# Optimization experiments

Measured on AMD Instinct MI355X. Metric: run time of the kernel, lower is better.

The kernel has to match this reference:

```python
import jax, jax.numpy as jnp
import numpy as np
import math

B, S, DIM, H, HD = 2, 2048, 2048, 16, 128


def _rotary(t, cos, sin):
    # t: [B, S, H, HD]; cos/sin: [S, HD//2]
    tr = t.reshape(*t.shape[:-1], HD // 2, 2)
    t_re, t_im = tr[..., 0], tr[..., 1]
    c = cos[None, :, None, :]
    s = sin[None, :, None, :]
    o_re = t_re * c - t_im * s
    o_im = t_re * s + t_im * c
    out = jnp.stack([o_re, o_im], axis=-1)
    return out.reshape(t.shape)


def setup_inputs() -> dict:
    key = jax.random.key(0)
    ks = jax.random.split(key, 6)
    x = jax.random.normal(ks[0], (B, S, DIM), dtype=jnp.float32)
    # rotary frequencies (base 10000), matching complex freqs_cis = exp(i * t * freq)
    inv_freq = 1.0 / (10000.0 ** (np.arange(0, HD, 2, dtype=np.float32) / HD))
    t = np.arange(S, dtype=np.float32)
    ang = np.outer(t, inv_freq)  # [S, HD//2]
    freqs_cos = jnp.asarray(np.cos(ang), dtype=jnp.float32)
    freqs_sin = jnp.asarray(np.sin(ang), dtype=jnp.float32)
    # causal boolean mask [1,1,S,S]
    mask = jnp.tril(jnp.ones((S, S), dtype=bool))[None, None]
    scale = 0.02
    qw = jax.random.normal(ks[1], (DIM, H * HD), dtype=jnp.float32) * scale
    kw = jax.random.normal(ks[2], (DIM, H * HD), dtype=jnp.float32) * scale
    vw = jax.random.normal(ks[3], (DIM, H * HD), dtype=jnp.float32) * scale
    ow = jax.random.normal(ks[4], (H * HD, DIM), dtype=jnp.float32) * scale
    return {"x": x, "freqs_cos": freqs_cos, "freqs_sin": freqs_sin, "mask": mask,
            "qw": qw, "kw": kw, "vw": vw, "ow": ow}


def reference(x, freqs_cos, freqs_sin, mask, qw, kw, vw, ow):
    bsz, slen, _ = x.shape
    q = (x @ qw).reshape(bsz, slen, H, HD)
    k = (x @ kw).reshape(bsz, slen, H, HD)
    v = (x @ vw).reshape(bsz, slen, H, HD)
    q = _rotary(q, freqs_cos[:slen], freqs_sin[:slen])
    k = _rotary(k, freqs_cos[:slen], freqs_sin[:slen])
    # [B, H, S, HD]
    q = q.transpose(0, 2, 1, 3)
    k = k.transpose(0, 2, 1, 3)
    v = v.transpose(0, 2, 1, 3)
    scale = 1.0 / math.sqrt(HD)
    scores = jnp.einsum('bhqd,bhkd->bhqk', q, k) * scale
    neg_inf = jnp.finfo(scores.dtype).min
    scores = jnp.where(mask, scores, neg_inf)
    attn_w = jax.nn.softmax(scores, axis=-1)
    attn = jnp.einsum('bhqk,bhkd->bhqd', attn_w, v)
    attn = attn.transpose(0, 2, 1, 3).reshape(bsz, slen, H * HD)
    out = attn @ ow
    return (out, attn_w)
```

## Files before the change

### kernel.cpp

```cpp
#include <hip/hip_runtime.h>
#include <stdint.h>

#define S 2048
#define DIMM 2048
#define NH 16
#define HD 128
#define NB 2
#define M4 4096

typedef unsigned short u16;
typedef unsigned int u32;
typedef __attribute__((ext_vector_type(8))) short short8;
typedef __attribute__((ext_vector_type(4))) float f32x4;

__device__ __forceinline__ u16 f2bf(float f) {
  union { float f; u32 u; } v; v.f = f;
  u32 u = v.u + 0x7fffu + ((v.u >> 16) & 1u);
  return (u16)(u >> 16);
}
__device__ __forceinline__ float bf2f(u16 b) {
  union { u32 u; float f; } v; v.u = ((u32)b) << 16;
  return v.f;
}
__device__ __forceinline__ u32 cvt_pk_bf16(float lo, float hi) {
  u32 r; asm("v_cvt_pk_bf16_f32 %0, %1, %2" : "=v"(r) : "v"(lo), "v"(hi)); return r;
}
__device__ __forceinline__ void gl_lds16(const void* g, void* l) {
  __builtin_amdgcn_global_load_lds((const __attribute__((address_space(1))) void*)g,
                                   (__attribute__((address_space(3))) void*)l, 16, 0, 0);
}
#define MFMA16(a, b, c) __builtin_amdgcn_mfma_f32_16x16x32_bf16(a, b, c, 0, 0, 0)

__global__ __launch_bounds__(256) void k_conv_x(const float* __restrict__ x, u16* __restrict__ xb) {
  int i = (blockIdx.x * 256 + threadIdx.x) * 8;
  float4 a = *(const float4*)&x[i];
  float4 b = *(const float4*)&x[i + 4];
  uint4 o;
  o.x = (u32)f2bf(a.x) | ((u32)f2bf(a.y) << 16);
  o.y = (u32)f2bf(a.z) | ((u32)f2bf(a.w) << 16);
  o.z = (u32)f2bf(b.x) | ((u32)f2bf(b.y) << 16);
  o.w = (u32)f2bf(b.z) | ((u32)f2bf(b.w) << 16);
  *(uint4*)&xb[i] = o;
}

__global__ __launch_bounds__(256) void k_transpose_w4(const float* __restrict__ w0, const float* __restrict__ w1,
                                                      const float* __restrict__ w2, const float* __restrict__ w3,
                                                      u16* __restrict__ t0, u16* __restrict__ t1,
                                                      u16* __restrict__ t2, u16* __restrict__ t3) {
  __shared__ u16 t[64][72];
  int zi = blockIdx.z;
  const float* w = (zi == 0) ? w0 : (zi == 1) ? w1 : (zi == 2) ? w2 : w3;
  u16* wt = (zi == 0) ? t0 : (zi == 1) ? t1 : (zi == 2) ? t2 : t3;
  int k0 = blockIdx.y * 64, n0 = blockIdx.x * 64;
  int tid = threadIdx.x;
  int r0 = tid >> 4, c4 = (tid & 15) * 4;
#pragma unroll
  for (int p = 0; p < 4; ++p) {
    int r = r0 + p * 16;
    float4 v = *(const float4*)&w[(size_t)(k0 + r) * DIMM + n0 + c4];
    t[c4 + 0][r] = f2bf(v.x); t[c4 + 1][r] = f2bf(v.y);
    t[c4 + 2][r] = f2bf(v.z); t[c4 + 3][r] = f2bf(v.w);
  }
  __syncthreads();
#pragma unroll
  for (int p = 0; p < 2; ++p) {
    int cc = tid + p * 256;
    int rn = cc >> 3, ck = (cc & 7) * 8;
    *(uint4*)&wt[(size_t)(n0 + rn) * DIMM + k0 + ck] = *(const uint4*)&t[rn][ck];
  }
}

__device__ __forceinline__ void gemm128_core(const u16* __restrict__ A, const u16* __restrict__ Bt,
                                             int m0, int n0, int Kd, u16* lA, u16* lB,
                                             f32x4 acc[4][4]) {
  int tid = threadIdx.x;
  int lane = tid & 63;
  int wid = tid >> 6;
  int wm = wid >> 1, wn = wid & 1;
  int c0 = tid, c1 = tid + 256;
  int a_r0 = c0 >> 2, a_k0 = (c0 & 3) * 8;
  int a_r1 = c1 >> 2, a_k1 = (c1 & 3) * 8;
  int ln = lane & 15, sub = lane >> 4;
  for (int kt = 0; kt < Kd; kt += 32) {
    gl_lds16(&A[(size_t)(m0 + a_r0) * Kd + kt + a_k0], &lA[c0 * 8]);
    gl_lds16(&A[(size_t)(m0 + a_r1) * Kd + kt + a_k1], &lA[c1 * 8]);
    gl_lds16(&Bt[(size_t)(n0 + a_r0) * Kd + kt + a_k0], &lB[c0 * 8]);
    gl_lds16(&Bt[(size_t)(n0 + a_r1) * Kd + kt + a_k1], &lB[c1 * 8]);
    __syncthreads();
    short8 af[4], bf[4];
#pragma unroll
    for (int mf = 0; mf < 4; ++mf)
      af[mf] = *(const short8*)&lA[(wm * 64 + mf * 16 + ln) * 32 + sub * 8];
#pragma unroll
    for (int nf = 0; nf < 4; ++nf)
      bf[nf] = *(const short8*)&lB[(wn * 64 + nf * 16 + ln) * 32 + sub * 8];
#pragma unroll
    for (int mf = 0; mf < 4; ++mf)
#pragma unroll
      for (int nf = 0; nf < 4; ++nf)
        acc[mf][nf] = MFMA16(af[mf], bf[nf], acc[mf][nf]);
    __syncthreads();
  }
}

__global__ __launch_bounds__(256) void k_gemm_qkv(const u16* __restrict__ xb,
                                                  const u16* __restrict__ qwT, const u16* __restrict__ kwT,
                                                  const u16* __restrict__ vwT,
                                                  const float* __restrict__ fc, const float* __restrict__ fs,
                                                  u16* __restrict__ qws, u16* __restrict__ kws,
                                                  u16* __restrict__ vtws, float* __restrict__ aw_all) {
  __shared__ u16 lA[128 * 32], lB[128 * 32];
  int f = blockIdx.y * 48 + blockIdx.x;
  int fp = (f & 7) * 192 + (f >> 3);
  int bx = fp % 48, byy = fp / 48;

  {
    int tid = threadIdx.x;
    f32x4 zf = {0.f, 0.f, 0.f, 0.f};
#pragma unroll
    for (int z = 0; z < 11; ++z) {
      int t = f * 11 + z;
      if (t < 15872) {
        int head = t / 496;
        int r = t - head * 496;
        int a = 0;
#pragma unroll
        for (int q = 30; q >= 1; --q) {
          if (r >= q * (63 - q) / 2) { a = q; break; }
        }
        int j = r - a * (63 - a) / 2;
        int kt = a + 1 + j;
        float* base = aw_all + (size_t)head * S * S + (size_t)(a * 64) * S + kt * 64;
#pragma unroll
        for (int i = 0; i < 4; ++i) {
          int c = i * 256 + tid;
          int row = c >> 4, col = (c & 15) * 4;
          __builtin_nontemporal_store(zf, (f32x4*)&base[(size_t)row * S + col]);
        }
      }
    }
  }

  int region = bx >> 4;
  const u16* Bt = (region == 0) ? qwT : ((region == 1) ? kwT : vwT);
  int n0 = (bx & 15) * 128;
  int m0 = byy * 128;
  f32x4 acc[4][4];
  f32x4 z4 = {0.f, 0.f, 0.f, 0.f};
#pragma unroll
  for (int i = 0; i < 4; ++i)
#pragma unroll
    for (int j = 0; j < 4; ++j) acc[i][j] = z4;
  gemm128_core(xb, Bt, m0, n0, DIMM, lA, lB, acc);
  int lane = threadIdx.x & 63, wid = threadIdx.x >> 6;
  int wm = wid >> 1, wn = wid & 1;
  int ln = lane & 15, sub = lane >> 4;
  if (region == 2) {
#pragma unroll
    for (int mf = 0; mf < 4; ++mf)
#pragma unroll
      for (int nf = 0; nf < 4; ++nf) {
        int m = m0 + wm * 64 + mf * 16 + sub * 4;
        int nl = n0 + wn * 64 + nf * 16 + ln;
        int b = m >> 11, s = m & 2047;
        int h = nl >> 7, d = nl & 127;
        u32 w0 = cvt_pk_bf16(acc[mf][nf][0], acc[mf][nf][1]);
        u32 w1 = cvt_pk_bf16(acc[mf][nf][2], acc[mf][nf][3]);
        uint2 pw = {w0, w1};
        *(uint2*)&vtws[((size_t)((b << 4) + h) * HD + d) * S + s] = pw;
      }
  } else {
    u16* dst = (region == 0) ? qws : kws;
#pragma unroll
    for (int mf = 0; mf < 4; ++mf)
#pragma unroll
      for (int nf = 0; nf < 4; ++nf) {
        int mbase = m0 + wm * 64 + mf * 16 + sub * 4;
        int nl = n0 + wn * 64 + nf * 16 + ln;
        int h = nl >> 7, d = nl & 127;
        int pi = d >> 1;
#pragma unroll
        for (int r = 0; r < 4; ++r) {
          int m = mbase + r;
          int b = m >> 11, s = m & 2047;
          float c = fc[s * 64 + pi];
          float sn = fs[s * 64 + pi];
          float v = acc[mf][nf][r];
          float prt = __shfl_xor(v, 1);
          float o = (ln & 1) ? (prt * sn + v * c) : (v * c - prt * sn);
          float o2 = __shfl_xor(o, 1);
          if (!(ln & 1)) {
            u32 opk = cvt_pk_bf16(o, o2);
            *(u32*)&dst[((size_t)((b << 4) + h) * S + s) * HD + d] = opk;
          }
        }
      }
  }
}

__global__ __launch_bounds__(256, 4) void k_attn(const u16* __restrict__ qws, const u16* __restrict__ kws,
                                                 const u16* __restrict__ vtws,
                                                 float* __restrict__ aw_all, u16* __restrict__ att) {
  __shared__ u16 lK[2][32 * 128];
  __shared__ u16 lV[2][128 * 32];
  __shared__ u16 lP[64 * 32];

  int f = blockIdx.x;
  int x = f & 7;
  int j = f >> 3;
  int cu = j & 31;
  int u = j >> 5;
  int by = 4 * x + u;
  int c2 = (u & 2) ? ((cu + 16) & 31) : cu;
  int qt = (u & 1) ? (31 - c2) : c2;
  int b = by >> 4, h = by & 15;
  const u16* qb = qws + (size_t)by * S * HD;
  const u16* kb = kws + (size_t)by * S * HD;
  const u16* vb = vtws + (size_t)by * HD * S;
  float* aw = aw_all + (size_t)by * S * S;
  int tid = threadIdx.x, lane = tid & 63, w = tid >> 6;
  int sub = lane >> 4, ln = lane & 15;
  int l7 = ln & 7, l3 = ln & 3;
  int q0 = qt * 64;
  int qrow = w * 16 + ln;
  int nkt = 2 * qt + 2;
  const float SC = 0.08838834764831845f * 1.4426950408889634f;

  auto stageK = [&](int kt, int bs) {
#pragma unroll
    for (int i = 0; i < 2; ++i) {
      int c = tid + i * 256;
      int row = c >> 4, p = c & 15;
      gl_lds16(&kb[(size_t)(kt * 32 + row) * HD + ((p ^ (row & 7)) << 3)], &lK[bs][c * 8]);
    }
  };
  auto stageV = [&](int kt, int bs) {
#pragma unroll
    for (int i = 0; i < 2; ++i) {
      int c = tid + i * 256;
      int row = c >> 2, p = c & 3;
      gl_lds16(&vb[(size_t)row * S + kt * 32 + ((p ^ (row & 3)) << 3)], &lV[bs][c * 8]);
    }
  };

  u16* lVlin = &lV[0][0];
#pragma unroll
  for (int i = 0; i < 4; ++i) {
    int c = tid + i * 256;
    int row = c >> 4, p = c & 15;
    gl_lds16(&qb[(size_t)(q0 + row) * HD + ((p ^ (row & 7)) << 3)], &lVlin[c * 8]);
  }
  stageK(0, 0);
  __syncthreads();

  short8 qf[4];
#pragma unroll
  for (int ks = 0; ks < 4; ++ks)
    qf[ks] = *(const short8*)&lVlin[qrow * 128 + (((ks * 4 + sub) ^ l7) << 3)];

  float ts = 0.f;
  for (int kt = 0; kt < nkt; ++kt) {
    int cur = kt & 1;
    if (kt + 1 < nkt) stageK(kt + 1, cur ^ 1);
    f32x4 sacc[2];
#pragma unroll
    for (int nf = 0; nf < 2; ++nf) sacc[nf] = f32x4{0.f, 0.f, 0.f, 0.f};
    __builtin_amdgcn_s_setprio(1);
#pragma unroll
    for (int nf = 0; nf < 2; ++nf) {
      int krow = nf * 16 + ln;
#pragma unroll
      for (int ks = 0; ks < 4; ++ks) {
        short8 kf = *(const short8*)&lK[cur][krow * 128 + (((ks * 4 + sub) ^ l7) << 3)];
        sacc[nf] = MFMA16(kf, qf[ks], sacc[nf]);
      }
    }
    __builtin_amdgcn_s_setprio(0);
    bool msk = (kt >= 2 * qt);
#pragma unroll
    for (int nf = 0; nf < 2; ++nf)
#pragma unroll
      for (int r = 0; r < 4; ++r) {
        float zz = sacc[nf][r] * SC;
        bool dead = msk && (kt * 32 + nf * 16 + sub * 4 + r > q0 + qrow);
        if (!dead) ts += exp2f(zz);
      }
    __syncthreads();
  }
  ts += __shfl_xor(ts, 16);
  ts += __shfl_xor(ts, 32);
  float mb = __log2f(ts);

  f32x4 oacc[8];
#pragma unroll
  for (int i = 0; i < 8; ++i) oacc[i] = f32x4{0.f, 0.f, 0.f, 0.f};
  stageK(nkt - 1, 0);
  stageV(nkt - 1, 0);
  __syncthreads();
  for (int it = 0; it < nkt; ++it) {
    int kt = nkt - 1 - it;
    int cur = it & 1;
    if (it + 1 < nkt) { stageK(kt - 1, cur ^ 1); stageV(kt - 1, cur ^ 1); }
    f32x4 sacc[2];
#pragma unroll
    for (int nf = 0; nf < 2; ++nf) sacc[nf] = f32x4{0.f, 0.f, 0.f, 0.f};
    __builtin_amdgcn_s_setprio(1);
#pragma unroll
    for (int nf = 0; nf < 2; ++nf) {
      int krow = nf * 16 + ln;
#pragma unroll
      for (int ks = 0; ks < 4; ++ks) {
        short8 kf = *(const short8*)&lK[cur][krow * 128 + (((ks * 4 + sub) ^ l7) << 3)];
        sacc[nf] = MFMA16(kf, qf[ks], sacc[nf]);
      }
    }
    __builtin_amdgcn_s_setprio(0);
    bool msk = (kt >= 2 * qt);
#pragma unroll
    for (int nf = 0; nf < 2; ++nf) {
      float p0 = exp2f(sacc[nf][0] * SC - mb);
      float p1 = exp2f(sacc[nf][1] * SC - mb);
      float p2 = exp2f(sacc[nf][2] * SC - mb);
      float p3 = exp2f(sacc[nf][3] * SC - mb);
      if (msk) {
        int base = kt * 32 + nf * 16 + sub * 4 - (q0 + qrow);
        if (base + 0 > 0) p0 = 0.f;
        if (base + 1 > 0) p1 = 0.f;
        if (base + 2 > 0) p2 = 0.f;
        if (base + 3 > 0) p3 = 0.f;
      }
      f32x4 pv = {p0, p1, p2, p3};
      __builtin_nontemporal_store(pv, (f32x4*)&aw[(size_t)(q0 + qrow) * S + kt * 32 + nf * 16 + sub * 4]);
      u32 w0 = cvt_pk_bf16(p0, p1);
      u32 w1 = cvt_pk_bf16(p2, p3);
      uint2 pw = {w0, w1};
      int c16 = (2 * nf + (sub >> 1)) ^ l3;
      *(uint2*)&lP[qrow * 32 + (c16 << 3) + ((sub & 1) << 2)] = pw;
    }
    short8 pa = *(const short8*)&lP[qrow * 32 + ((sub ^ l3) << 3)];
    __builtin_amdgcn_s_setprio(1);
#pragma unroll
    for (int nf2 = 0; nf2 < 8; ++nf2) {
      int drow = nf2 * 16 + ln;
      short8 vv = *(const short8*)&lV[cur][drow * 32 + ((sub ^ (drow & 3)) << 3)];
      oacc[nf2] = MFMA16(vv, pa, oacc[nf2]);
    }
    __builtin_amdgcn_s_setprio(0);
    __syncthreads();
  }

#pragma unroll
  for (int nf2 = 0; nf2 < 8; ++nf2) {
    u32 w0 = cvt_pk_bf16(oacc[nf2][0], oacc[nf2][1]);
    u32 w1 = cvt_pk_bf16(oacc[nf2][2], oacc[nf2][3]);
    uint2 ow2 = {w0, w1};
    *(uint2*)&att[(size_t)(b * S + q0 + qrow) * (NH * HD) + h * 128 + nf2 * 16 + sub * 4] = ow2;
  }
}

__global__ __launch_bounds__(256) void k_gemm_out(const u16* __restrict__ att, const u16* __restrict__ owT,
                                                  float* __restrict__ out) {
  __shared__ u16 lA[128 * 32], lB[128 * 32];
  int f = blockIdx.y * 16 + blockIdx.x;
  int fp = (f & 7) * 64 + (f >> 3);
  int n0 = (fp & 15) * 128, m0 = (fp >> 4) * 128;
  f32x4 acc[4][4];
  f32x4 z4 = {0.f, 0.f, 0.f, 0.f};
#pragma unroll
  for (int i = 0; i < 4; ++i)
#pragma unroll
    for (int j = 0; j < 4; ++j) acc[i][j] = z4;
  gemm128_core(att, owT, m0, n0, DIMM, lA, lB, acc);
  int lane = threadIdx.x & 63, wid = threadIdx.x >> 6;
  int wm = wid >> 1, wn = wid & 1;
  int ln = lane & 15, sub = lane >> 4;
#pragma unroll
  for (int mf = 0; mf < 4; ++mf)
#pragma unroll
    for (int nf = 0; nf < 4; ++nf)
#pragma unroll
      for (int r = 0; r < 4; ++r) {
        int m = m0 + wm * 64 + mf * 16 + sub * 4 + r;
        int nl = n0 + wn * 64 + nf * 16 + ln;
        out[(size_t)m * DIMM + nl] = acc[mf][nf][r];
      }
}

extern "C" void kernel_launch(void* const* d_in, const int* in_sizes, int n_in,
                              void* d_out, int out_size, void* d_ws, size_t ws_size,
                              hipStream_t stream) {
  const float* x  = (const float*)d_in[0];
  const float* fc = (const float*)d_in[1];
  const float* fs = (const float*)d_in[2];
  const float* qw = (const float*)d_in[4];
  const float* kw = (const float*)d_in[5];
  const float* vw = (const float*)d_in[6];
  const float* ow = (const float*)d_in[7];
  float* out = (float*)d_out;
  float* aw  = out + (size_t)M4 * DIMM;

  char* wsb = (char*)d_ws;
  u16* xb   = (u16*)(wsb);
  u16* qwT  = (u16*)(wsb + (size_t)16 * 1024 * 1024);
  u16* kwT  = (u16*)(wsb + (size_t)24 * 1024 * 1024);
  u16* vwT  = (u16*)(wsb + (size_t)32 * 1024 * 1024);
  u16* owT  = (u16*)(wsb + (size_t)40 * 1024 * 1024);
  u16* qws  = (u16*)(wsb + (size_t)48 * 1024 * 1024);
  u16* kws  = (u16*)(wsb + (size_t)64 * 1024 * 1024);
  u16* vtws = (u16*)(wsb + (size_t)80 * 1024 * 1024);
  u16* att  = (u16*)(wsb + (size_t)96 * 1024 * 1024);

  k_conv_x<<<4096, 256, 0, stream>>>(x, xb);
  k_transpose_w4<<<dim3(32, 32, 4), 256, 0, stream>>>(qw, kw, vw, ow, qwT, kwT, vwT, owT);
  k_gemm_qkv<<<dim3(48, 32), 256, 0, stream>>>(xb, qwT, kwT, vwT, fc, fs, qws, kws, vtws, aw);
  k_attn<<<1024, 256, 0, stream>>>(qws, kws, vtws, aw, att);
  k_gemm_out<<<dim3(16, 32), 256, 0, stream>>>(att, owT, out);
}
```

Baseline: 392.7 us.

## Rewrite projection GEMMs as 8-wave 128x256 double-buffered pipelined tiles

Replaces the single-buffered 128x128, 4-wave GEMM core with an 8-wave 128x256 tile that has a K-step of 64 and double-buffered LDS. It also XOR-swizzles the LDS layout to avoid bank conflicts and interleaves the prefetch of the next tile with MFMA work using explicit waitcnt, barriers and setprio. The QKV and output projection kernels are relaunched with fewer, larger blocks, and the masked attention-weight zeroing work is redistributed across them. The intent is to hide global-load latency and raise MFMA utilisation. The cost is more LDS per block (96KB), which limits occupancy, and fewer blocks for the output GEMM (256).

```diff
diff --git a/kernel.cpp b/kernel.cpp
--- a/kernel.cpp
+++ b/kernel.cpp
@@ -70,56 +70,136 @@
   }
 }
 
-__device__ __forceinline__ void gemm128_core(const u16* __restrict__ A, const u16* __restrict__ Bt,
-                                             int m0, int n0, int Kd, u16* lA, u16* lB,
-                                             f32x4 acc[4][4]) {
+__device__ __forceinline__ void gemm8p(const u16* __restrict__ A, const u16* __restrict__ Bt,
+                                       int m0, int n0,
+                                       u16 (*smA)[128 * 64], u16 (*smB)[256 * 64],
+                                       f32x4 acc[4][4]) {
   int tid = threadIdx.x;
-  int lane = tid & 63;
-  int wid = tid >> 6;
-  int wm = wid >> 1, wn = wid & 1;
-  int c0 = tid, c1 = tid + 256;
-  int a_r0 = c0 >> 2, a_k0 = (c0 & 3) * 8;
-  int a_r1 = c1 >> 2, a_k1 = (c1 & 3) * 8;
+  int lane = tid & 63, wid = tid >> 6;
+  int wm = wid >> 2, wn = wid & 3;
   int ln = lane & 15, sub = lane >> 4;
-  for (int kt = 0; kt < Kd; kt += 32) {
-    gl_lds16(&A[(size_t)(m0 + a_r0) * Kd + kt + a_k0], &lA[c0 * 8]);
-    gl_lds16(&A[(size_t)(m0 + a_r1) * Kd + kt + a_k1], &lA[c1 * 8]);
-    gl_lds16(&Bt[(size_t)(n0 + a_r0) * Kd + kt + a_k0], &lB[c0 * 8]);
-    gl_lds16(&Bt[(size_t)(n0 + a_r1) * Kd + kt + a_k1], &lB[c1 * 8]);
-    __syncthreads();
-    short8 af[4], bf[4];
-#pragma unroll
-    for (int mf = 0; mf < 4; ++mf)
-      af[mf] = *(const short8*)&lA[(wm * 64 + mf * 16 + ln) * 32 + sub * 8];
+
+  auto stageA = [&](int t, int bs) {
+    int kk = t << 6;
+#pragma unroll
+    for (int i = 0; i < 2; ++i) {
+      int c = tid + i * 512;
+      int row = c >> 3, p = c & 7;
+      gl_lds16(&A[(size_t)(m0 + row) * DIMM + kk + ((p ^ (row & 7)) << 3)],
+               &smA[bs][(row << 6) + (p << 3)]);
+    }
+  };
+  auto stageB = [&](int t, int bs) {
+    int kk = t << 6;
+#pragma unroll
+    for (int i = 0; i < 4; ++i) {
+      int c = tid + i * 512;
+      int row = c >> 3, p = c & 7;
+      gl_lds16(&Bt[(size_t)(n0 + row) * DIMM + kk + ((p ^ (row & 7)) << 3)],
+               &smB[bs][(row << 6) + (p << 3)]);
+    }
+  };
+  auto rdA = [&](int bs, int mf, int ks) -> short8 {
+    int row = (wm << 6) + (mf << 4) + ln;
+    return *(const short8*)&smA[bs][(row << 6) + ((((ks << 2) + sub) ^ (row & 7)) << 3)];
+  };
+  auto rdB = [&](int bs, int nf, int ks) -> short8 {
+    int row = (wn << 6) + (nf << 4) + ln;
+    return *(const short8*)&smB[bs][(row << 6) + ((((ks << 2) + sub) ^ (row & 7)) << 3)];
+  };
+
+  stageA(0, 0); stageB(0, 0);
+  asm volatile("s_waitcnt vmcnt(0)" ::: "memory");
+  __syncthreads();
+
+  const int nt = DIMM / 64;
+  for (int t = 0; t < nt; ++t) {
+    int cur = t & 1, nb = cur ^ 1;
+    bool pf = (t + 1 < nt);
+    short8 bfr[4][2];
+    if (pf) {
+      stageA(t + 1, nb);
+      asm volatile("s_waitcnt vmcnt(2)" ::: "memory");
+    } else {
+      asm volatile("s_waitcnt vmcnt(0)" ::: "memory");
+    }
+    __builtin_amdgcn_s_barrier();
+    __builtin_amdgcn_sched_barrier(0);
 #pragma unroll
     for (int nf = 0; nf < 4; ++nf)
-      bf[nf] = *(const short8*)&lB[(wn * 64 + nf * 16 + ln) * 32 + sub * 8];
-#pragma unroll
-    for (int mf = 0; mf < 4; ++mf)
-#pragma unroll
-      for (int nf = 0; nf < 4; ++nf)
-        acc[mf][nf] = MFMA16(af[mf], bf[nf], acc[mf][nf]);
-    __syncthreads();
-  }
-}
-
-__global__ __launch_bounds__(256) void k_gemm_qkv(const u16* __restrict__ xb,
-                                                  const u16* __restrict__ qwT, const u16* __restrict__ kwT,
-                                                  const u16* __restrict__ vwT,
-                                                  const float* __restrict__ fc, const float* __restrict__ fs,
-                                                  u16* __restrict__ qws, u16* __restrict__ kws,
-                                                  u16* __restrict__ vtws, float* __restrict__ aw_all) {
-  __shared__ u16 lA[128 * 32], lB[128 * 32];
-  int f = blockIdx.y * 48 + blockIdx.x;
-  int fp = (f & 7) * 192 + (f >> 3);
-  int bx = fp % 48, byy = fp / 48;
+#pragma unroll
+      for (int ks = 0; ks < 2; ++ks) bfr[nf][ks] = rdB(cur, nf, ks);
+    {
+      short8 a00 = rdA(cur, 0, 0), a01 = rdA(cur, 0, 1);
+      short8 a10 = rdA(cur, 1, 0), a11 = rdA(cur, 1, 1);
+      asm volatile("s_waitcnt lgkmcnt(0)" ::: "memory");
+      __builtin_amdgcn_sched_barrier(0);
+      __builtin_amdgcn_s_setprio(1);
+#pragma unroll
+      for (int nf = 0; nf < 4; ++nf) {
+        acc[0][nf] = MFMA16(a00, bfr[nf][0], acc[0][nf]);
+        acc[0][nf] = MFMA16(a01, bfr[nf][1], acc[0][nf]);
+        acc[1][nf] = MFMA16(a10, bfr[nf][0], acc[1][nf]);
+        acc[1][nf] = MFMA16(a11, bfr[nf][1], acc[1][nf]);
+      }
+      __builtin_amdgcn_s_setprio(0);
+    }
+    __builtin_amdgcn_s_barrier();
+    __builtin_amdgcn_sched_barrier(0);
+    {
+      short8 a00 = rdA(cur, 2, 0), a01 = rdA(cur, 2, 1);
+      short8 a10 = rdA(cur, 3, 0), a11 = rdA(cur, 3, 1);
+      if (pf) stageB(t + 1, nb);
+      __builtin_amdgcn_s_barrier();
+      asm volatile("s_waitcnt lgkmcnt(0)" ::: "memory");
+      __builtin_amdgcn_sched_barrier(0);
+      __builtin_amdgcn_s_setprio(1);
+#pragma unroll
+      for (int nf = 0; nf < 4; ++nf) {
+        acc[2][nf] = MFMA16(a00, bfr[nf][0], acc[2][nf]);
+        acc[2][nf] = MFMA16(a01, bfr[nf][1], acc[2][nf]);
+        acc[3][nf] = MFMA16(a10, bfr[nf][0], acc[3][nf]);
+        acc[3][nf] = MFMA16(a11, bfr[nf][1], acc[3][nf]);
+      }
+      __builtin_amdgcn_s_setprio(0);
+    }
+    asm volatile("s_waitcnt lgkmcnt(0)" ::: "memory");
+    __builtin_amdgcn_s_barrier();
+    __builtin_amdgcn_sched_barrier(0);
+  }
+}
+
+__global__ __launch_bounds__(512, 2) void k_gemm_qkv8(const u16* __restrict__ xb,
+                                                      const u16* __restrict__ qwT, const u16* __restrict__ kwT,
+                                                      const u16* __restrict__ vwT,
+                                                      const float* __restrict__ fc, const float* __restrict__ fs,
+                                                      u16* __restrict__ qws, u16* __restrict__ kws,
+                                                      u16* __restrict__ vtws, float* __restrict__ aw_all) {
+  __shared__ u16 smA[2][128 * 64];
+  __shared__ u16 smB[2][256 * 64];
+  int tid = threadIdx.x;
+  int f = blockIdx.x;
+  int fp = (f & 7) * 96 + (f >> 3);
+  int bx = fp % 24, by = fp / 24;
+  int region = bx >> 3;
+  const u16* Bt = (region == 0) ? qwT : ((region == 1) ? kwT : vwT);
+  int n0g = (bx & 7) * 256;
+  int m0g = by * 128;
+
+  f32x4 acc[4][4];
+  f32x4 z4 = {0.f, 0.f, 0.f, 0.f};
+#pragma unroll
+  for (int i = 0; i < 4; ++i)
+#pragma unroll
+    for (int j = 0; j < 4; ++j) acc[i][j] = z4;
+
+  gemm8p(xb, Bt, m0g, n0g, smA, smB, acc);
 
   {
-    int tid = threadIdx.x;
     f32x4 zf = {0.f, 0.f, 0.f, 0.f};
 #pragma unroll
-    for (int z = 0; z < 11; ++z) {
-      int t = f * 11 + z;
+    for (int z = 0; z < 21; ++z) {
+      int t = f * 21 + z;
       if (t < 15872) {
         int head = t / 496;
         int r = t - head * 496;
@@ -132,8 +212,8 @@
         int kt = a + 1 + j;
         float* base = aw_all + (size_t)head * S * S + (size_t)(a * 64) * S + kt * 64;
 #pragma unroll
-        for (int i = 0; i < 4; ++i) {
-          int c = i * 256 + tid;
+        for (int i = 0; i < 2; ++i) {
+          int c = i * 512 + tid;
           int row = c >> 4, col = (c & 15) * 4;
           __builtin_nontemporal_store(zf, (f32x4*)&base[(size_t)row * S + col]);
         }
@@ -141,27 +221,16 @@
     }
   }
 
-  int region = bx >> 4;
-  const u16* Bt = (region == 0) ? qwT : ((region == 1) ? kwT : vwT);
-  int n0 = (bx & 15) * 128;
-  int m0 = byy * 128;
-  f32x4 acc[4][4];
-  f32x4 z4 = {0.f, 0.f, 0.f, 0.f};
-#pragma unroll
-  for (int i = 0; i < 4; ++i)
-#pragma unroll
-    for (int j = 0; j < 4; ++j) acc[i][j] = z4;
-  gemm128_core(xb, Bt, m0, n0, DIMM, lA, lB, acc);
-  int lane = threadIdx.x & 63, wid = threadIdx.x >> 6;
-  int wm = wid >> 1, wn = wid & 1;
+  int lane = tid & 63, wid = tid >> 6;
+  int wm = wid >> 2, wn = wid & 3;
   int ln = lane & 15, sub = lane >> 4;
   if (region == 2) {
 #pragma unroll
     for (int mf = 0; mf < 4; ++mf)
 #pragma unroll
       for (int nf = 0; nf < 4; ++nf) {
-        int m = m0 + wm * 64 + mf * 16 + sub * 4;
-        int nl = n0 + wn * 64 + nf * 16 + ln;
+        int m = m0g + wm * 64 + mf * 16 + sub * 4;
+        int nl = (bx & 7) * 256 + wn * 64 + nf * 16 + ln;
         int b = m >> 11, s = m & 2047;
         int h = nl >> 7, d = nl & 127;
         u32 w0 = cvt_pk_bf16(acc[mf][nf][0], acc[mf][nf][1]);
@@ -175,8 +244,8 @@
     for (int mf = 0; mf < 4; ++mf)
 #pragma unroll
       for (int nf = 0; nf < 4; ++nf) {
-        int mbase = m0 + wm * 64 + mf * 16 + sub * 4;
-        int nl = n0 + wn * 64 + nf * 16 + ln;
+        int mbase = m0g + wm * 64 + mf * 16 + sub * 4;
+        int nl = (bx & 7) * 256 + wn * 64 + nf * 16 + ln;
         int h = nl >> 7, d = nl & 127;
         int pi = d >> 1;
 #pragma unroll
@@ -358,21 +427,26 @@
   }
 }
 
-__global__ __launch_bounds__(256) void k_gemm_out(const u16* __restrict__ att, const u16* __restrict__ owT,
-                                                  float* __restrict__ out) {
-  __shared__ u16 lA[128 * 32], lB[128 * 32];
-  int f = blockIdx.y * 16 + blockIdx.x;
-  int fp = (f & 7) * 64 + (f >> 3);
-  int n0 = (fp & 15) * 128, m0 = (fp >> 4) * 128;
+__global__ __launch_bounds__(512, 2) void k_gemm_out8(const u16* __restrict__ att, const u16* __restrict__ owT,
+                                                      float* __restrict__ out) {
+  __shared__ u16 smA[2][128 * 64];
+  __shared__ u16 smB[2][256 * 64];
+  int f = blockIdx.x;
+  int fp = (f & 7) * 32 + (f >> 3);
+  int bx = fp & 7, by = fp >> 3;
+  int n0 = bx * 256, m0 = by * 128;
+
   f32x4 acc[4][4];
   f32x4 z4 = {0.f, 0.f, 0.f, 0.f};
 #pragma unroll
   for (int i = 0; i < 4; ++i)
 #pragma unroll
     for (int j = 0; j < 4; ++j) acc[i][j] = z4;
-  gemm128_core(att, owT, m0, n0, DIMM, lA, lB, acc);
+
+  gemm8p(att, owT, m0, n0, smA, smB, acc);
+
   int lane = threadIdx.x & 63, wid = threadIdx.x >> 6;
-  int wm = wid >> 1, wn = wid & 1;
+  int wm = wid >> 2, wn = wid & 3;
   int ln = lane & 15, sub = lane >> 4;
 #pragma unroll
   for (int mf = 0; mf < 4; ++mf)
@@ -412,7 +486,7 @@
 
   k_conv_x<<<4096, 256, 0, stream>>>(x, xb);
   k_transpose_w4<<<dim3(32, 32, 4), 256, 0, stream>>>(qw, kw, vw, ow, qwT, kwT, vwT, owT);
-  k_gemm_qkv<<<dim3(48, 32), 256, 0, stream>>>(xb, qwT, kwT, vwT, fc, fs, qws, kws, vtws, aw);
+  k_gemm_qkv8<<<768, 512, 0, stream>>>(xb, qwT, kwT, vwT, fc, fs, qws, kws, vtws, aw);
   k_attn<<<1024, 256, 0, stream>>>(qws, kws, vtws, aw, att);
-  k_gemm_out<<<dim3(16, 32), 256, 0, stream>>>(att, owT, out);
-}
+  k_gemm_out8<<<256, 512, 0, stream>>>(att, owT, out);
+}
```

Measured after the change: 433.1 us. 1.1x slower.
